# Optimization experiments

Measured on AMD Instinct MI355X. Metric: run time of the kernel, lower is better.

The kernel has to match this reference:

```python
import jax, jax.numpy as jnp
import numpy as np

PROPOSAL_COUNT = 1000
NMS_THRESHOLD = 0.7
PRE_NMS_LIMIT = 6000
RPN_BBOX_STD_DEV = np.array([0.1, 0.1, 0.2, 0.2], dtype=np.float32)
B, N = 4, 261888


def setup_inputs() -> dict:
    key = jax.random.key(0)
    k1, k2, k3, k4, k5, k6 = jax.random.split(key, 6)
    logits = jax.random.normal(k1, (B, N, 2), dtype=jnp.float32)
    rpn_probs = jax.nn.softmax(logits, axis=-1)
    rpn_deltas = jax.random.normal(k2, (B, N, 4), dtype=jnp.float32) * 0.1
    # anchors as valid normalized boxes (y1,x1,y2,x2)
    cy = jax.random.uniform(k3, (B, N), dtype=jnp.float32)
    cx = jax.random.uniform(k4, (B, N), dtype=jnp.float32)
    h = jax.random.uniform(k5, (B, N), dtype=jnp.float32) * 0.2 + 0.02
    w = jax.random.uniform(k6, (B, N), dtype=jnp.float32) * 0.2 + 0.02
    anchors = jnp.stack([cy - 0.5 * h, cx - 0.5 * w, cy + 0.5 * h, cx + 0.5 * w], axis=-1)
    return {"rpn_probs": rpn_probs, "rpn_deltas": rpn_deltas, "anchors": anchors}


def apply_box_deltas(boxes, deltas):
    # boxes, deltas: [K, 4]
    h = boxes[:, 2] - boxes[:, 0]
    w = boxes[:, 3] - boxes[:, 1]
    cy = boxes[:, 0] + 0.5 * h + deltas[:, 0] * h
    cx = boxes[:, 1] + 0.5 * w + deltas[:, 1] * w
    h = h * jnp.exp(deltas[:, 2])
    w = w * jnp.exp(deltas[:, 3])
    y1 = cy - 0.5 * h
    x1 = cx - 0.5 * w
    return jnp.stack([y1, x1, y1 + h, x1 + w], axis=1)


def _iou_matrix(boxes):
    # boxes: [K, 4] -> IoU [K, K]
    y1, x1, y2, x2 = jnp.split(boxes, 4, axis=1)  # each [K,1]
    area = (y2 - y1) * (x2 - x1)
    ih = jnp.maximum(jnp.minimum(y2, y2.T) - jnp.maximum(y1, y1.T), 0.0)
    iw = jnp.maximum(jnp.minimum(x2, x2.T) - jnp.maximum(x1, x1.T), 0.0)
    inter = ih * iw
    return inter / (area + area.T - inter + 1e-8)


def nms_single(boxes, scores):
    # boxes: [K,4] already sorted by descending score; greedy NMS like tf.image.non_max_suppression
    K = boxes.shape[0]
    iou = _iou_matrix(jax.lax.stop_gradient(boxes))

    def body(i, suppressed):
        keep_i = jnp.logical_not(suppressed[i])
        new = jnp.where(keep_i, jnp.logical_or(suppressed, iou[i] > NMS_THRESHOLD), suppressed)
        return new.at[i].set(suppressed[i])

    suppressed = jax.lax.fori_loop(0, K, body, jnp.zeros((K,), dtype=bool))
    keep = jnp.logical_not(suppressed)
    # stable: kept indices first (already score-sorted), then take top proposal_count
    order = jnp.argsort(jnp.where(keep, jnp.arange(K), K))
    sel = order[:PROPOSAL_COUNT]
    valid = jnp.arange(PROPOSAL_COUNT) < jnp.sum(keep)
    return boxes[sel] * valid[:, None].astype(boxes.dtype)  # zero-pad like tf.pad


def reference(rpn_probs, rpn_deltas, anchors):
    scores = rpn_probs[:, :, 1]                              # [B, N] fg scores
    deltas = rpn_deltas * RPN_BBOX_STD_DEV.reshape(1, 1, 4)  # [B, N, 4]
    k = min(PRE_NMS_LIMIT, anchors.shape[1])
    top_scores, ix = jax.lax.top_k(scores, k)                # sorted descending
    deltas_k = jnp.take_along_axis(deltas, ix[:, :, None], axis=1)   # [B, k, 4]
    anchors_k = jnp.take_along_axis(anchors, ix[:, :, None], axis=1)  # [B, k, 4]
    boxes = jax.vmap(apply_box_deltas)(anchors_k, deltas_k)
    boxes = jnp.clip(boxes, 0.0, 1.0)                        # window [0,0,1,1]
    return jax.vmap(nms_single)(boxes, top_scores)           # [B, proposal_count, 4]
```

## Files before the change

kernel.cpp:

```cpp
#include <hip/hip_runtime.h>

typedef unsigned int u32;
typedef unsigned long long u64;

#define BB 4
#define NN 261888
#define KSEL 6000
#define CAP 8192
#define PC 1000
#define NMS_THR 0.7f
#define NW 94
#define NWP 96
#define NR (NW*64)
#define COLSPLIT 6

#define HB 31
#define CHUNK_H (NN/HB)
#define HITER (CHUNK_H/256)
#define CB 93
#define CHUNK_C (NN/CB)
#define CITER (CHUNK_C/256)

#define HIST1_OFF 0
#define HIST2_OFF (BB*2048)
#define SEL_OFF   (BB*2048*2)
#define CNT_OFF   (BB*2048*2 + BB*4)
#define ZERO_WORDS (BB*2048*2 + BB*4 + BB*32)

__global__ void k_zero(u32* ws) {
    int i = blockIdx.x * 256 + threadIdx.x;
    if (i < ZERO_WORDS) ws[i] = 0u;
}

__global__ void k_hist1(const float2* __restrict__ probs2, u32* __restrict__ hist1) {
    __shared__ u32 lh[2048];
    int b = blockIdx.y;
    size_t base = (size_t)b * NN + (size_t)blockIdx.x * CHUNK_H;
    for (int j = threadIdx.x; j < 2048; j += 256) lh[j] = 0u;
    __syncthreads();
    #pragma unroll 4
    for (int it = 0; it < HITER; ++it) {
        float2 p = probs2[base + it * 256 + threadIdx.x];
        atomicAdd(&lh[__float_as_uint(p.y) >> 21], 1u);
    }
    __syncthreads();
    for (int j = threadIdx.x; j < 2048; j += 256) {
        u32 c = lh[j];
        if (c) atomicAdd(&hist1[b * 2048 + j], c);
    }
}

__global__ void k_sel1(const u32* __restrict__ hist1, u32* __restrict__ sel) {
    __shared__ u32 gsum[256];
    __shared__ u32 lh[2048];
    int b = blockIdx.x;
    int t = threadIdx.x;
    u32 s = 0;
    #pragma unroll
    for (int j = 0; j < 8; ++j) {
        u32 v = hist1[b * 2048 + 2047 - (t * 8 + j)];
        lh[t * 8 + j] = v;
        s += v;
    }
    gsum[t] = s;
    __syncthreads();
    if (t == 0) {
        u32 cum = 0;
        for (int g = 0; g < 256; ++g) {
            if (cum + gsum[g] >= (u32)KSEL) {
                for (int j = 0; j < 8; ++j) {
                    u32 c = lh[g * 8 + j];
                    if (cum + c >= (u32)KSEL) {
                        sel[b * 4 + 0] = (u32)(2047 - (g * 8 + j));
                        sel[b * 4 + 1] = cum;
                        break;
                    }
                    cum += c;
                }
                break;
            }
            cum += gsum[g];
        }
    }
}

__global__ void k_hist2(const float2* __restrict__ probs2, const u32* __restrict__ sel,
                        u32* __restrict__ hist2) {
    int b = blockIdx.y;
    u32 b1 = sel[b * 4 + 0];
    size_t base = (size_t)b * NN + (size_t)blockIdx.x * CHUNK_H;
    #pragma unroll 4
    for (int it = 0; it < HITER; ++it) {
        float2 p = probs2[base + it * 256 + threadIdx.x];
        u32 key = __float_as_uint(p.y);
        if ((key >> 21) == b1) atomicAdd(&hist2[b * 2048 + ((key >> 10) & 2047u)], 1u);
    }
}

__global__ void k_sel2(const u32* __restrict__ hist2, u32* __restrict__ sel) {
    __shared__ u32 gsum[256];
    __shared__ u32 lh[2048];
    int b = blockIdx.x;
    int t = threadIdx.x;
    u32 s = 0;
    #pragma unroll
    for (int j = 0; j < 8; ++j) {
        u32 v = hist2[b * 2048 + 2047 - (t * 8 + j)];
        lh[t * 8 + j] = v;
        s += v;
    }
    gsum[t] = s;
    __syncthreads();
    if (t == 0) {
        u32 cum = sel[b * 4 + 1];
        u32 b1 = sel[b * 4 + 0];
        for (int g = 0; g < 256; ++g) {
            if (cum + gsum[g] >= (u32)KSEL) {
                for (int j = 0; j < 8; ++j) {
                    cum += lh[g * 8 + j];
                    if (cum >= (u32)KSEL) {
                        sel[b * 4 + 2] = (b1 << 11) | (u32)(2047 - (g * 8 + j));
                        break;
                    }
                }
                break;
            }
            cum += gsum[g];
        }
    }
}

__global__ void k_compact(const float2* __restrict__ probs2, const u32* __restrict__ sel,
                          u32* __restrict__ candCount, u64* __restrict__ cand) {
    __shared__ u32 wsum[4];
    __shared__ u32 blkBase;
    int b = blockIdx.y;
    int tid = threadIdx.x;
    int wave = tid >> 6, lane = tid & 63;
    u32 base = (u32)blockIdx.x * CHUNK_C;
    u32 thr = sel[b * 4 + 2];

    u32 keys[CITER];
    u32 cnt = 0;
    #pragma unroll
    for (int it = 0; it < CITER; ++it) {
        float2 p = probs2[(size_t)b * NN + base + it * 256 + tid];
        u32 key = __float_as_uint(p.y);
        keys[it] = key;
        cnt += ((key >> 10) >= thr) ? 1u : 0u;
    }
    #pragma unroll
    for (int off = 32; off; off >>= 1) cnt += __shfl_down(cnt, off);
    if (lane == 0) wsum[wave] = cnt;
    __syncthreads();
    if (tid == 0) {
        u32 w0 = wsum[0], w1 = wsum[1], w2 = wsum[2], w3 = wsum[3];
        u32 tot = w0 + w1 + w2 + w3;
        wsum[0] = 0; wsum[1] = w0; wsum[2] = w0 + w1; wsum[3] = w0 + w1 + w2;
        blkBase = tot ? atomicAdd(&candCount[b * 32], tot) : 0u;
    }
    __syncthreads();
    u32 run = blkBase + wsum[wave];
    u64* cb = cand + (size_t)b * CAP;
    #pragma unroll
    for (int it = 0; it < CITER; ++it) {
        u32 key = keys[it];
        bool pred = (key >> 10) >= thr;
        u64 m = __ballot(pred);
        if (pred) {
            u32 pos = run + (u32)__popcll(m & ((1ull << lane) - 1ull));
            u32 gi = base + it * 256 + tid;
            if (pos < CAP) cb[pos] = ((u64)key << 32) | (u32)(~gi);
        }
        run += (u32)__popcll(m);
    }
}

__global__ __launch_bounds__(512) void k_rank(const u64* __restrict__ cand,
                                              const u32* __restrict__ candCount,
                                              u64* __restrict__ sorted) {
    __shared__ u64 keys[CAP];
    int b = blockIdx.y;
    int tid = threadIdx.x;
    int cnt = (int)candCount[b * 32];
    if (cnt > CAP) cnt = CAP;
    const u64* cb = cand + (size_t)b * CAP;
    for (int j = tid; j < CAP; j += 512)
        keys[j] = (j < cnt) ? cb[j] : 0ull;
    __syncthreads();
    int r = blockIdx.x * 512 + tid;
    if (r >= cnt) return;
    u64 my = keys[r];
    int cnt16 = (cnt + 15) & ~15;
    int rank = 0;
    for (int j = 0; j < cnt16; j += 16) {
        #pragma unroll
        for (int u = 0; u < 16; ++u)
            rank += (keys[j + u] > my) ? 1 : 0;
    }
    if (rank < KSEL) sorted[(size_t)b * KSEL + rank] = my;
}

__global__ void k_decode(const u64* __restrict__ sorted,
                         const float4* __restrict__ anchors, const float4* __restrict__ deltas,
                         float4* __restrict__ boxes) {
    int b = blockIdx.y;
    int t = blockIdx.x * 256 + threadIdx.x;
    if (t >= KSEL) return;
    u64 sk = sorted[(size_t)b * KSEL + t];
    u32 idx = ~(u32)(sk & 0xFFFFFFFFull);
    if (idx >= NN) idx = NN - 1;
    float4 a = anchors[(size_t)b * NN + idx];
    float4 d = deltas[(size_t)b * NN + idx];
    float dy = __fmul_rn(d.x, 0.1f);
    float dx = __fmul_rn(d.y, 0.1f);
    float dh = __fmul_rn(d.z, 0.2f);
    float dw = __fmul_rn(d.w, 0.2f);
    float h  = __fsub_rn(a.z, a.x);
    float w  = __fsub_rn(a.w, a.y);
    float cy = __fadd_rn(__fadd_rn(a.x, __fmul_rn(0.5f, h)), __fmul_rn(dy, h));
    float cx = __fadd_rn(__fadd_rn(a.y, __fmul_rn(0.5f, w)), __fmul_rn(dx, w));
    float h2 = __fmul_rn(h, expf(dh));
    float w2 = __fmul_rn(w, expf(dw));
    float y1 = __fsub_rn(cy, __fmul_rn(0.5f, h2));
    float x1 = __fsub_rn(cx, __fmul_rn(0.5f, w2));
    float y2 = __fadd_rn(y1, h2);
    float x2 = __fadd_rn(x1, w2);
    y1 = fminf(fmaxf(y1, 0.0f), 1.0f);
    x1 = fminf(fmaxf(x1, 0.0f), 1.0f);
    y2 = fminf(fmaxf(y2, 0.0f), 1.0f);
    x2 = fminf(fmaxf(x2, 0.0f), 1.0f);
    float4 out;
    out.x = y1; out.y = x1; out.z = y2; out.w = x2;
    boxes[(size_t)b * KSEL + t] = out;
}

__global__ void k_sortgather(const u64* __restrict__ cand, const u32* __restrict__ candCount,
                             const float4* __restrict__ anchors, const float4* __restrict__ deltas,
                             float4* __restrict__ boxes) {
    __shared__ u64 s[CAP];
    int b = blockIdx.x;
    int tid = threadIdx.x;
    u32 cnt = candCount[b * 32];
    if (cnt > CAP) cnt = CAP;
    for (int j = tid; j < CAP; j += 1024)
        s[j] = (j < (int)cnt) ? cand[(size_t)b * CAP + j] : 0ull;
    __syncthreads();
    for (int k = 2; k <= CAP; k <<= 1) {
        for (int j = k >> 1; j > 0; j >>= 1) {
            for (int idx = tid; idx < CAP; idx += 1024) {
                int l = idx ^ j;
                if (l > idx) {
                    u64 a = s[idx], c = s[l];
                    bool dir = ((idx & k) == 0);
                    if ((a < c) == dir) { s[idx] = c; s[l] = a; }
                }
            }
            __syncthreads();
        }
    }
    for (int t = tid; t < KSEL; t += 1024) {
        u64 sk = s[t];
        u32 idx = ~(u32)(sk & 0xFFFFFFFFull);
        float4 a = anchors[(size_t)b * NN + idx];
        float4 d = deltas[(size_t)b * NN + idx];
        float dy = __fmul_rn(d.x, 0.1f);
        float dx = __fmul_rn(d.y, 0.1f);
        float dh = __fmul_rn(d.z, 0.2f);
        float dw = __fmul_rn(d.w, 0.2f);
        float h  = __fsub_rn(a.z, a.x);
        float w  = __fsub_rn(a.w, a.y);
        float cy = __fadd_rn(__fadd_rn(a.x, __fmul_rn(0.5f, h)), __fmul_rn(dy, h));
        float cx = __fadd_rn(__fadd_rn(a.y, __fmul_rn(0.5f, w)), __fmul_rn(dx, w));
        float h2 = __fmul_rn(h, expf(dh));
        float w2 = __fmul_rn(w, expf(dw));
        float y1 = __fsub_rn(cy, __fmul_rn(0.5f, h2));
        float x1 = __fsub_rn(cx, __fmul_rn(0.5f, w2));
        float y2 = __fadd_rn(y1, h2);
        float x2 = __fadd_rn(x1, w2);
        y1 = fminf(fmaxf(y1, 0.0f), 1.0f);
        x1 = fminf(fmaxf(x1, 0.0f), 1.0f);
        y2 = fminf(fmaxf(y2, 0.0f), 1.0f);
        x2 = fminf(fmaxf(x2, 0.0f), 1.0f);
        float4 out;
        out.x = y1; out.y = x1; out.z = y2; out.w = x2;
        boxes[(size_t)b * KSEL + t] = out;
    }
}

__global__ __launch_bounds__(256) void k_iou(const float4* __restrict__ boxes,
                                             u64* __restrict__ mask) {
    __shared__ float4 colBox[4][64];
    __shared__ float  colArea[4][64];
    int b = blockIdx.z;
    int rblk = blockIdx.x;
    int r0 = rblk * 64;
    int tid = threadIdx.x;
    int wave = tid >> 6, lane = tid & 63;
    const float4* B4 = boxes + (size_t)b * KSEL;

    int r = r0 + lane;
    float4 rb;
    if (r < KSEL) rb = B4[r];
    else { rb.x = 2.0f; rb.y = 2.0f; rb.z = 3.0f; rb.w = 3.0f; }
    float ra = __fmul_rn(__fsub_rn(rb.z, rb.x), __fsub_rn(rb.w, rb.y));

    const double M0 = 0.5 * ((double)__uint_as_float(0x3F333333u)
                           + (double)__uint_as_float(0x3F333334u));
    u64* Mb = mask + (size_t)b * NR * NWP;

    for (int jw = rblk + blockIdx.y * 4 + wave; jw < NW; jw += 4 * COLSPLIT) {
        int j = jw * 64 + lane;
        float4 cbx;
        if (j < KSEL) cbx = B4[j];
        else { cbx.x = 2.0f; cbx.y = 2.0f; cbx.z = 3.0f; cbx.w = 3.0f; }
        colBox[wave][lane] = cbx;
        colArea[wave][lane] = __fmul_rn(__fsub_rn(cbx.z, cbx.x), __fsub_rn(cbx.w, cbx.y));
        asm volatile("" ::: "memory");

        u64 word = 0ull;
        #pragma unroll
        for (int c = 0; c < 64; ++c) {
            float4 cb = colBox[wave][c];
            float ca = colArea[wave][c];
            float ih = fmaxf(__fsub_rn(fminf(rb.z, cb.z), fmaxf(rb.x, cb.x)), 0.0f);
            float iw = fmaxf(__fsub_rn(fminf(rb.w, cb.w), fmaxf(rb.y, cb.y)), 0.0f);
            float inter = __fmul_rn(ih, iw);
            float denom = __fadd_rn(__fsub_rn(__fadd_rn(ra, ca), inter), 1e-8f);
            bool pred = ((double)inter >= M0 * (double)denom);
            word |= ((u64)pred) << c;
        }
        Mb[(size_t)(r0 + lane) * NWP + jw] = word;
        asm volatile("" ::: "memory");
    }
}

__device__ __forceinline__ u64 readlane64(u64 v, int lane) {
    u32 lo = (u32)__builtin_amdgcn_readlane((int)(u32)v, lane);
    u32 hi = (u32)__builtin_amdgcn_readlane((int)(u32)(v >> 32), lane);
    return ((u64)hi << 32) | (u64)lo;
}
__device__ __forceinline__ u64 rfl64(u64 v) {
    u32 lo = (u32)__builtin_amdgcn_readfirstlane((int)(u32)v);
    u32 hi = (u32)__builtin_amdgcn_readfirstlane((int)(u32)(v >> 32));
    return ((u64)hi << 32) | (u64)lo;
}

__global__ __launch_bounds__(512) void k_reduce(const u64* __restrict__ mask,
                                                const float4* __restrict__ boxes,
                                                float* __restrict__ outp) {
    __shared__ u64 pub[8];
    __shared__ u64 kbLDS;
    __shared__ u32 kLDS;
    __shared__ u32 keptIdx[PC];
    int b = blockIdx.x;
    int tid = threadIdx.x;
    int wv = tid >> 6, lane = tid & 63;
    const u64* M = mask + (size_t)b * NR * NWP;
    const float4* B4 = boxes + (size_t)b * KSEL;
    int lp = lane < 46 ? lane : 46;
    u64 rwA = 0ull, rwB = 0ull;
    int k = 0, kprev = 0;

    if (tid < 8) pub[tid] = 0ull;

    ulonglong2 cur[8], mid[8], nxt[8];
    u64 dgCur, dgMid, dgNxt;
    #pragma unroll
    for (int r = 0; r < 8; ++r) {
        cur[r] = *(const ulonglong2*)(M + (size_t)(wv * 8 + r) * NWP + 2 * lp);
        mid[r] = *(const ulonglong2*)(M + (size_t)(64 + wv * 8 + r) * NWP + 2 * lp);
    }
    dgCur = M[(size_t)lane * NWP + 0];
    dgMid = M[(size_t)(64 + lane) * NWP + 1];
    __syncthreads();

    for (int g = 0; g < NW; ++g) {
        int gn = (g + 2 < NW) ? g + 2 : NW - 1;
        #pragma unroll
        for (int r = 0; r < 8; ++r)
            nxt[r] = *(const ulonglong2*)(M + (size_t)(gn * 64 + wv * 8 + r) * NWP + 2 * lp);
        dgNxt = M[(size_t)(gn * 64 + lane) * NWP + gn];

        if (wv == 0) {
            u64 rem = pub[0] | pub[1] | pub[2] | pub[3] | pub[4] | pub[5] | pub[6] | pub[7];
            rem = rfl64(rem);
            int remaining = KSEL - g * 64;
            u64 valid = (remaining >= 64) ? ~0ull : ((1ull << remaining) - 1ull);
            u64 todo = ~rem & valid;
            u64 kb0 = 0ull;
            int k0 = k;
            while (todo && k0 < PC) {
                int i = (int)__builtin_ctzll(todo);
                kb0 |= (1ull << i);
                ++k0;
                u64 drow = __ballot((dgCur >> i) & 1ull);
                todo &= ~(drow | (1ull << i));
            }
            if ((kb0 >> lane) & 1ull) {
                int rank = kprev + (int)__popcll(kb0 & ((1ull << lane) - 1ull));
                keptIdx[rank] = (u32)(g * 64 + lane);
            }
            kprev = k0;
            if (lane == 0) { kbLDS = kb0; kLDS = (u32)k0; }
        }
        __syncthreads();
        u64 kb = kbLDS;
        k = (int)kLDS;

        #pragma unroll
        for (int r = 0; r < 8; ++r)
            if ((kb >> (wv * 8 + r)) & 1ull) { rwA |= cur[r].x; rwB |= cur[r].y; }

        if (k >= PC || g == NW - 1) break;

        int nw_ = g + 1;
        u64 wpub = (nw_ & 1) ? readlane64(rwB, nw_ >> 1) : readlane64(rwA, nw_ >> 1);
        if (lane == 0) pub[wv] = wpub;

        #pragma unroll
        for (int r = 0; r < 8; ++r) { cur[r] = mid[r]; mid[r] = nxt[r]; }
        dgCur = dgMid; dgMid = dgNxt;
        __syncthreads();
    }
    __syncthreads();

    float4* O = (float4*)outp + (size_t)b * PC;
    for (int t = tid; t < PC; t += 512) {
        float4 v; v.x = 0.0f; v.y = 0.0f; v.z = 0.0f; v.w = 0.0f;
        if (t < k) v = B4[keptIdx[t]];
        O[t] = v;
    }
}

__global__ void k_nms(const float4* __restrict__ boxes, float* __restrict__ outp) {
    __shared__ float4 chunk[512];
    __shared__ float4 keptBox[PC];
    __shared__ float  keptArea[PC];
    __shared__ u32    flag[2];
    int b = blockIdx.x;
    int tid = threadIdx.x;
    const float4* B4 = boxes + (size_t)b * KSEL;

    if (tid < 2) flag[tid] = 0u;
    for (int j = tid; j < 512; j += 256) chunk[j] = B4[j];
    __syncthreads();

    int kc = 0;
    for (int i = 0; i < KSEL && kc < PC; ++i) {
        int ci = i & 511;
        if (ci == 0 && i != 0) {
            for (int j = tid; j < 512 && (i + j) < KSEL; j += 256) chunk[j] = B4[i + j];
            __syncthreads();
        }
        float4 cb = chunk[ci];
        float careaV = __fmul_rn(__fsub_rn(cb.z, cb.x), __fsub_rn(cb.w, cb.y));
        bool sup = false;
        for (int t = tid; t < kc; t += 256) {
            float4 kb2 = keptBox[t];
            float ih = fmaxf(__fsub_rn(fminf(cb.z, kb2.z), fmaxf(cb.x, kb2.x)), 0.0f);
            float iw = fmaxf(__fsub_rn(fminf(cb.w, kb2.w), fmaxf(cb.y, kb2.y)), 0.0f);
            float inter = __fmul_rn(ih, iw);
            float denom = __fadd_rn(__fsub_rn(__fadd_rn(careaV, keptArea[t]), inter), 1e-8f);
            if (__fdiv_rn(inter, denom) > NMS_THR) sup = true;
        }
        int p = i & 1;
        if (sup) flag[p] = 1u;
        if (tid == 0) flag[p ^ 1] = 0u;
        __syncthreads();
        if (flag[p] == 0u) {
            if (tid == 0) { keptBox[kc] = cb; keptArea[kc] = careaV; }
            kc++;
        }
        __syncthreads();
    }

    float4* out4 = (float4*)outp + (size_t)b * PC;
    for (int r = tid; r < PC; r += 256) {
        float4 v;
        if (r < kc) v = keptBox[r];
        else { v.x = 0.0f; v.y = 0.0f; v.z = 0.0f; v.w = 0.0f; }
        out4[r] = v;
    }
}

extern "C" void kernel_launch(void* const* d_in, const int* in_sizes, int n_in,
                              void* d_out, int out_size, void* d_ws, size_t ws_size,
                              hipStream_t stream) {
    const float* probs   = (const float*)d_in[0];
    const float* deltas  = (const float*)d_in[1];
    const float* anchors = (const float*)d_in[2];
    float* outp = (float*)d_out;

    u32* ws32 = (u32*)d_ws;
    u32* hist1 = ws32 + HIST1_OFF;
    u32* hist2 = ws32 + HIST2_OFF;
    u32* sel   = ws32 + SEL_OFF;
    u32* candCount = ws32 + CNT_OFF;
    u64* cand   = (u64*)(ws32 + ZERO_WORDS);
    u64* sorted = cand + (size_t)BB * CAP;
    float* boxesF = (float*)(sorted + (size_t)BB * KSEL);
    float4* boxes = (float4*)boxesF;
    u64* mask = (u64*)(boxesF + (size_t)BB * KSEL * 4);

    size_t needed = (size_t)ZERO_WORDS * 4 + (size_t)BB * CAP * 8 + (size_t)BB * KSEL * 8
                  + (size_t)BB * KSEL * 16 + (size_t)BB * NR * NWP * 8;

    hipLaunchKernelGGL(k_zero, dim3((ZERO_WORDS + 255) / 256), dim3(256), 0, stream, ws32);
    hipLaunchKernelGGL(k_hist1, dim3(HB, BB), dim3(256), 0, stream, (const float2*)probs, hist1);
    hipLaunchKernelGGL(k_sel1, dim3(BB), dim3(256), 0, stream, hist1, sel);
    hipLaunchKernelGGL(k_hist2, dim3(HB, BB), dim3(256), 0, stream, (const float2*)probs, sel, hist2);
    hipLaunchKernelGGL(k_sel2, dim3(BB), dim3(256), 0, stream, hist2, sel);
    hipLaunchKernelGGL(k_compact, dim3(CB, BB), dim3(256), 0, stream, (const float2*)probs, sel, candCount, cand);
    if (ws_size >= needed) {
        hipLaunchKernelGGL(k_rank, dim3(CAP / 512, BB), dim3(512), 0, stream, cand, candCount, sorted);
        hipLaunchKernelGGL(k_decode, dim3((KSEL + 255) / 256, BB), dim3(256), 0, stream,
                           sorted, (const float4*)anchors, (const float4*)deltas, boxes);
        hipLaunchKernelGGL(k_iou, dim3(NW, COLSPLIT, BB), dim3(256), 0, stream, boxes, mask);
        hipLaunchKernelGGL(k_reduce, dim3(BB), dim3(512), 0, stream, mask, boxes, outp);
    } else {
        hipLaunchKernelGGL(k_sortgather, dim3(BB), dim3(1024), 0, stream,
                           cand, candCount, (const float4*)anchors, (const float4*)deltas, boxes);
        hipLaunchKernelGGL(k_nms, dim3(BB), dim3(256), 0, stream, boxes, outp);
    }
}
```

Measured before the change: 261.0 us.

## Split rank-counting across column chunks with atomic partial ranks and scatter pass

```diff
diff --git a/kernel.cpp b/kernel.cpp
--- a/kernel.cpp
+++ b/kernel.cpp
@@ -21,11 +21,15 @@
 #define CHUNK_C (NN/CB)
 #define CITER (CHUNK_C/256)
 
+#define CS 4
+#define CPS (CAP/CS)
+
 #define HIST1_OFF 0
 #define HIST2_OFF (BB*2048)
 #define SEL_OFF   (BB*2048*2)
 #define CNT_OFF   (BB*2048*2 + BB*4)
-#define ZERO_WORDS (BB*2048*2 + BB*4 + BB*32)
+#define RANK_OFF  (BB*2048*2 + BB*4 + BB*32)
+#define ZERO_WORDS (BB*2048*2 + BB*4 + BB*32 + BB*CAP)
 
 __global__ void k_zero(u32* ws) {
     int i = blockIdx.x * 256 + threadIdx.x;
@@ -178,27 +182,38 @@
 
 __global__ __launch_bounds__(512) void k_rank(const u64* __restrict__ cand,
                                               const u32* __restrict__ candCount,
-                                              u64* __restrict__ sorted) {
-    __shared__ u64 keys[CAP];
-    int b = blockIdx.y;
+                                              u32* __restrict__ rankArr) {
+    __shared__ u64 keys[CPS];
+    int b = blockIdx.z;
+    int c0 = blockIdx.y * CPS;
     int tid = threadIdx.x;
     int cnt = (int)candCount[b * 32];
     if (cnt > CAP) cnt = CAP;
     const u64* cb = cand + (size_t)b * CAP;
-    for (int j = tid; j < CAP; j += 512)
-        keys[j] = (j < cnt) ? cb[j] : 0ull;
+    for (int j = tid; j < CPS; j += 512)
+        keys[j] = (c0 + j < cnt) ? cb[c0 + j] : 0ull;
     __syncthreads();
     int r = blockIdx.x * 512 + tid;
     if (r >= cnt) return;
-    u64 my = keys[r];
-    int cnt16 = (cnt + 15) & ~15;
-    int rank = 0;
-    for (int j = 0; j < cnt16; j += 16) {
+    u64 my = cb[r];
+    u32 rank = 0;
+    for (int j = 0; j < CPS; j += 16) {
         #pragma unroll
         for (int u = 0; u < 16; ++u)
-            rank += (keys[j + u] > my) ? 1 : 0;
-    }
-    if (rank < KSEL) sorted[(size_t)b * KSEL + rank] = my;
+            rank += (keys[j + u] > my) ? 1u : 0u;
+    }
+    if (rank) atomicAdd(&rankArr[b * CAP + r], rank);
+}
+
+__global__ void k_scatter(const u64* __restrict__ cand, const u32* __restrict__ candCount,
+                          const u32* __restrict__ rankArr, u64* __restrict__ sorted) {
+    int b = blockIdx.y;
+    int p = blockIdx.x * 256 + threadIdx.x;
+    int cnt = (int)candCount[b * 32];
+    if (cnt > CAP) cnt = CAP;
+    if (p >= cnt) return;
+    u32 rank = rankArr[b * CAP + p];
+    if (rank < KSEL) sorted[(size_t)b * KSEL + rank] = cand[(size_t)b * CAP + p];
 }
 
 __global__ void k_decode(const u64* __restrict__ sorted,
@@ -497,6 +512,7 @@
     u32* hist2 = ws32 + HIST2_OFF;
     u32* sel   = ws32 + SEL_OFF;
     u32* candCount = ws32 + CNT_OFF;
+    u32* rankArr   = ws32 + RANK_OFF;
     u64* cand   = (u64*)(ws32 + ZERO_WORDS);
     u64* sorted = cand + (size_t)BB * CAP;
     float* boxesF = (float*)(sorted + (size_t)BB * KSEL);
@@ -513,7 +529,8 @@
     hipLaunchKernelGGL(k_sel2, dim3(BB), dim3(256), 0, stream, hist2, sel);
     hipLaunchKernelGGL(k_compact, dim3(CB, BB), dim3(256), 0, stream, (const float2*)probs, sel, candCount, cand);
     if (ws_size >= needed) {
-        hipLaunchKernelGGL(k_rank, dim3(CAP / 512, BB), dim3(512), 0, stream, cand, candCount, sorted);
+        hipLaunchKernelGGL(k_rank, dim3(CAP / 512, CS, BB), dim3(512), 0, stream, cand, candCount, rankArr);
+        hipLaunchKernelGGL(k_scatter, dim3(CAP / 256, BB), dim3(256), 0, stream, cand, candCount, rankArr, sorted);
         hipLaunchKernelGGL(k_decode, dim3((KSEL + 255) / 256, BB), dim3(256), 0, stream,
                            sorted, (const float4*)anchors, (const float4*)deltas, boxes);
         hipLaunchKernelGGL(k_iou, dim3(NW, COLSPLIT, BB), dim3(256), 0, stream, boxes, mask);
```

New measurement: 214.1 us. 1.22x faster.
